# Optimization experiments

Measured on AMD Instinct MI355X. Metric: run time of the kernel, lower is better.

Reference implementation:

```python
import jax, jax.numpy as jnp
import numpy as np

B, T, C, H = 4, 1024, 1024, 16
D = C // H
EPS = 1e-5


def _ln(x, g, b):
    mu = jnp.mean(x, axis=-1, keepdims=True)
    var = jnp.mean((x - mu) ** 2, axis=-1, keepdims=True)
    return (x - mu) * jax.lax.rsqrt(var + EPS) * g + b


def _attn(xq, xkv, wq, wk, wv, wo, bo, mask):
    # wq/wk/wv/wo: [C, C] (in, out). Dropout is identity in eval mode.
    Bq, Tq, _ = xq.shape
    Tk = xkv.shape[1]
    q = (xq @ wq).reshape(Bq, Tq, H, D)
    k = (xkv @ wk).reshape(Bq, Tk, H, D)
    v = (xkv @ wv).reshape(Bq, Tk, H, D)
    scores = jnp.einsum('bqhd,bkhd->bhqk', q, k) / jnp.sqrt(jnp.float32(D))
    if mask is not None:
        scores = jnp.where(mask == 0, -jnp.inf, scores)
    p = jax.nn.softmax(scores, axis=-1)
    out = jnp.einsum('bhqk,bkhd->bqhd', p, v).reshape(Bq, Tq, C)
    return out @ wo + bo


def setup_inputs() -> dict:
    key = jax.random.key(0)
    ks = jax.random.split(key, 20)
    s = 0.02
    inp = {
        'x': jax.random.normal(ks[0], (B, T, C), jnp.float32),
        'encoder_out': jax.random.normal(ks[1], (B, T, C), jnp.float32),
        'sa_wq': jax.random.normal(ks[2], (C, C), jnp.float32) * s,
        'sa_wk': jax.random.normal(ks[3], (C, C), jnp.float32) * s,
        'sa_wv': jax.random.normal(ks[4], (C, C), jnp.float32) * s,
        'sa_wo': jax.random.normal(ks[5], (C, C), jnp.float32) * s,
        'sa_bo': jnp.zeros((C,), jnp.float32),
        'ca_wq': jax.random.normal(ks[6], (C, C), jnp.float32) * s,
        'ca_wk': jax.random.normal(ks[7], (C, C), jnp.float32) * s,
        'ca_wv': jax.random.normal(ks[8], (C, C), jnp.float32) * s,
        'ca_wo': jax.random.normal(ks[9], (C, C), jnp.float32) * s,
        'ca_bo': jnp.zeros((C,), jnp.float32),
        'ff_w1': jax.random.normal(ks[10], (C, 4 * C), jnp.float32) * s,
        'ff_b1': jnp.zeros((4 * C,), jnp.float32),
        'ff_w2': jax.random.normal(ks[11], (4 * C, C), jnp.float32) * s,
        'ff_b2': jnp.zeros((C,), jnp.float32),
        'ln1_g': jnp.ones((C,), jnp.float32), 'ln1_b': jnp.zeros((C,), jnp.float32),
        'ln2_g': jnp.ones((C,), jnp.float32), 'ln2_b': jnp.zeros((C,), jnp.float32),
        'ln3_g': jnp.ones((C,), jnp.float32), 'ln3_b': jnp.zeros((C,), jnp.float32),
        'tgt_mask': jnp.tril(jnp.ones((T, T), jnp.int32))[None, None],  # [1,1,T,T] causal
        'src_mask': jnp.ones((B, 1, 1, T), jnp.int32),
    }
    return inp


def reference(x, encoder_out, sa_wq, sa_wk, sa_wv, sa_wo, sa_bo,
              ca_wq, ca_wk, ca_wv, ca_wo, ca_bo,
              ff_w1, ff_b1, ff_w2, ff_b2,
              ln1_g, ln1_b, ln2_g, ln2_b, ln3_g, ln3_b,
              tgt_mask, src_mask):
    # self-attention (masked) + residual
    x = x + _attn(_ln(x, ln1_g, ln1_b), _ln(x, ln1_g, ln1_b),
                  sa_wq, sa_wk, sa_wv, sa_wo, sa_bo, tgt_mask)
    # cross-attention + residual (only src_mask applied to scores)
    h = _ln(x, ln2_g, ln2_b)
    x = x + _attn(h, encoder_out, ca_wq, ca_wk, ca_wv, ca_wo, ca_bo, src_mask)
    # FFN + residual
    h = _ln(x, ln3_g, ln3_b)
    x = x + (jax.nn.relu(h @ ff_w1 + ff_b1) @ ff_w2 + ff_b2)
    return x
```

## Files before the change

kernel.cpp:

```cpp
#include <hip/hip_runtime.h>

typedef __bf16 bf16_t;
typedef __bf16 bf16x4 __attribute__((ext_vector_type(4)));
typedef __bf16 bf16x8 __attribute__((ext_vector_type(8)));
typedef float  f32x4  __attribute__((ext_vector_type(4)));

#define LN_EPS 1e-5f

__device__ __forceinline__ void g2l16(const bf16_t* g, bf16_t* l) {
    __builtin_amdgcn_global_load_lds(
        (const __attribute__((address_space(1))) void*)g,
        (__attribute__((address_space(3))) void*)l, 16, 0, 0);
}

__global__ __launch_bounds__(256) void cvt_kernel(
    const float* __restrict__ x, bf16_t* __restrict__ y)
{
    int i = blockIdx.x * 256 + threadIdx.x;
    f32x4 v = ((const f32x4*)x)[i];
    bf16x4 o = { (bf16_t)v.x, (bf16_t)v.y, (bf16_t)v.z, (bf16_t)v.w };
    ((bf16x4*)y)[i] = o;
}

struct WTBatch { const float* src[8]; bf16_t* dst[8]; };

__global__ __launch_bounds__(256) void wt_batch_kernel(WTBatch p)
{
    const int K = 1024, N = 1024;
    const float* W = p.src[blockIdx.z];
    bf16_t* Wt = p.dst[blockIdx.z];
    __shared__ float ts[64][65];
    const int n0 = blockIdx.x * 64, k0 = blockIdx.y * 64;
    const int tid = threadIdx.x;
#pragma unroll
    for (int it = 0; it < 4; ++it) {
        int f = tid + it * 256;
        int row = f >> 4, c4 = (f & 15) * 4;
        f32x4 v = *(const f32x4*)(W + (size_t)(k0 + row) * N + n0 + c4);
        ts[row][c4 + 0] = v.x; ts[row][c4 + 1] = v.y;
        ts[row][c4 + 2] = v.z; ts[row][c4 + 3] = v.w;
    }
    __syncthreads();
#pragma unroll
    for (int it = 0; it < 4; ++it) {
        int f = tid + it * 256;
        int nrow = f >> 4, k4 = (f & 15) * 4;
        bf16x4 o = { (bf16_t)ts[k4 + 0][nrow], (bf16_t)ts[k4 + 1][nrow],
                     (bf16_t)ts[k4 + 2][nrow], (bf16_t)ts[k4 + 3][nrow] };
        *(bf16x4*)(Wt + (size_t)(n0 + nrow) * K + k0 + k4) = o;
    }
}

__global__ __launch_bounds__(256) void wt_kernel(
    const float* __restrict__ W, bf16_t* __restrict__ Wt, int K, int N)
{
    __shared__ float ts[64][65];
    const int n0 = blockIdx.x * 64, k0 = blockIdx.y * 64;
    const int tid = threadIdx.x;
#pragma unroll
    for (int it = 0; it < 4; ++it) {
        int f = tid + it * 256;
        int row = f >> 4, c4 = (f & 15) * 4;
        f32x4 v = *(const f32x4*)(W + (size_t)(k0 + row) * N + n0 + c4);
        ts[row][c4 + 0] = v.x; ts[row][c4 + 1] = v.y;
        ts[row][c4 + 2] = v.z; ts[row][c4 + 3] = v.w;
    }
    __syncthreads();
#pragma unroll
    for (int it = 0; it < 4; ++it) {
        int f = tid + it * 256;
        int nrow = f >> 4, k4 = (f & 15) * 4;
        bf16x4 o = { (bf16_t)ts[k4 + 0][nrow], (bf16_t)ts[k4 + 1][nrow],
                     (bf16_t)ts[k4 + 2][nrow], (bf16_t)ts[k4 + 3][nrow] };
        *(bf16x4*)(Wt + (size_t)(n0 + nrow) * K + k0 + k4) = o;
    }
}

__global__ __launch_bounds__(256) void ln_kernel(
    const float* __restrict__ x, const float* __restrict__ g,
    const float* __restrict__ b, bf16_t* __restrict__ y)
{
    const int row = blockIdx.x;
    const int tid = threadIdx.x;
    const f32x4* xr = (const f32x4*)(x + (size_t)row * 1024);
    f32x4 v = xr[tid];
    float s  = v.x + v.y + v.z + v.w;
    float s2 = v.x*v.x + v.y*v.y + v.z*v.z + v.w*v.w;
#pragma unroll
    for (int off = 1; off < 64; off <<= 1) {
        s  += __shfl_xor(s,  off, 64);
        s2 += __shfl_xor(s2, off, 64);
    }
    __shared__ float ws_[4], ws2_[4];
    const int wave = tid >> 6, lane = tid & 63;
    if (lane == 0) { ws_[wave] = s; ws2_[wave] = s2; }
    __syncthreads();
    s  = ws_[0] + ws_[1] + ws_[2] + ws_[3];
    s2 = ws2_[0] + ws2_[1] + ws2_[2] + ws2_[3];
    const float mu   = s  * (1.0f/1024.0f);
    const float var  = s2 * (1.0f/1024.0f) - mu*mu;
    const float rstd = rsqrtf(var + LN_EPS);
    f32x4 gv = ((const f32x4*)g)[tid];
    f32x4 bv = ((const f32x4*)b)[tid];
    f32x4 o  = (v - mu) * rstd * gv + bv;
    bf16x4 ob = { (bf16_t)o.x, (bf16_t)o.y, (bf16_t)o.z, (bf16_t)o.w };
    ((bf16x4*)(y + (size_t)row * 1024))[tid] = ob;
}

template<int BN, int OUT_BF16, int HAS_BIAS, int DO_RELU, int HAS_RES>
__global__ __launch_bounds__(256) void gemm_bf16(
    const bf16_t* __restrict__ A, const bf16_t* __restrict__ Bt,
    const float* __restrict__ bias, const float* __restrict__ res,
    void* __restrict__ out, int M, int N, int K)
{
    constexpr int NT = BN / 32;
    __shared__ __align__(16) bf16_t As[2][128 * 32];
    __shared__ __align__(16) bf16_t Bs[2][BN * 32];

    const int tid  = threadIdx.x;
    const int wave = tid >> 6, lane = tid & 63;
    const int q    = lane >> 4, r = lane & 15;
    const int wm   = wave >> 1, wn = wave & 1;
    const int m0   = blockIdx.y * 128, n0 = blockIdx.x * BN;

    const int srow = lane >> 2;
    const int schk = (lane & 3) * 8;

    auto stage = [&](int buf, int kk) {
#pragma unroll
        for (int t = 0; t < 2; ++t) {
            int rowA = wave * 32 + t * 16;
            g2l16(A + (size_t)(m0 + rowA + srow) * K + kk + schk, &As[buf][rowA * 32]);
        }
        if constexpr (BN == 128) {
#pragma unroll
            for (int t = 0; t < 2; ++t) {
                int rowB = wave * 32 + t * 16;
                g2l16(Bt + (size_t)(n0 + rowB + srow) * K + kk + schk, &Bs[buf][rowB * 32]);
            }
        } else {
            int rowB = wave * 16;
            g2l16(Bt + (size_t)(n0 + rowB + srow) * K + kk + schk, &Bs[buf][rowB * 32]);
        }
    };

    f32x4 acc[4][NT] = {};
    stage(0, 0);

    for (int kk = 0; kk < K; kk += 32) {
        const int cur = (kk >> 5) & 1;
        __syncthreads();
        if (kk + 32 < K) stage(cur ^ 1, kk + 32);

        bf16x8 af[4], bf[NT];
#pragma unroll
        for (int i = 0; i < 4; ++i)
            af[i] = *(const bf16x8*)&As[cur][(wm * 64 + i * 16 + r) * 32 + q * 8];
#pragma unroll
        for (int j = 0; j < NT; ++j)
            bf[j] = *(const bf16x8*)&Bs[cur][(wn * 16 * NT + j * 16 + r) * 32 + q * 8];
#pragma unroll
        for (int i = 0; i < 4; ++i)
#pragma unroll
            for (int j = 0; j < NT; ++j)
                acc[i][j] = __builtin_amdgcn_mfma_f32_16x16x32_bf16(af[i], bf[j], acc[i][j], 0, 0, 0);
    }

#pragma unroll
    for (int i = 0; i < 4; ++i)
#pragma unroll
        for (int j = 0; j < NT; ++j)
#pragma unroll
            for (int e = 0; e < 4; ++e) {
                int row = m0 + wm * 64 + i * 16 + q * 4 + e;
                int col = n0 + wn * 16 * NT + j * 16 + r;
                float v = acc[i][j][e];
                if (HAS_BIAS) v += bias[col];
                if (DO_RELU)  v = v > 0.0f ? v : 0.0f;
                if (HAS_RES)  v += res[(size_t)row * N + col];
                if (OUT_BF16) ((bf16_t*)out)[(size_t)row * N + col] = (bf16_t)v;
                else          ((float*)out)[(size_t)row * N + col] = v;
            }
}

__global__ __launch_bounds__(256) void gemm_qkv3(
    const bf16_t* __restrict__ Aq, const bf16_t* __restrict__ Akv,
    const bf16_t* __restrict__ Wt3,
    bf16_t* __restrict__ outq, bf16_t* __restrict__ outk,
    bf16_t* __restrict__ vt)
{
    const int K = 1024;
    __shared__ __align__(16) bf16_t As[2][128 * 32];
    __shared__ __align__(16) bf16_t Bs[2][128 * 32];

    const int tid  = threadIdx.x;
    const int wave = tid >> 6, lane = tid & 63;
    const int q    = lane >> 4, r = lane & 15;
    const int wm   = wave >> 1, wn = wave & 1;
    const int m0   = blockIdx.y * 128, n0 = blockIdx.x * 128;
    const int grp  = blockIdx.x >> 3;
    const bf16_t* A = (grp == 0) ? Aq : Akv;

    const int srow = lane >> 2;
    const int schk = (lane & 3) * 8;

    auto stage = [&](int buf, int kk) {
#pragma unroll
        for (int t = 0; t < 2; ++t) {
            int row = wave * 32 + t * 16;
            g2l16(A   + (size_t)(m0 + row + srow) * K + kk + schk, &As[buf][row * 32]);
            g2l16(Wt3 + (size_t)(n0 + row + srow) * K + kk + schk, &Bs[buf][row * 32]);
        }
    };

    f32x4 acc[4][4] = {};
    stage(0, 0);

    for (int kk = 0; kk < K; kk += 32) {
        const int cur = (kk >> 5) & 1;
        __syncthreads();
        if (kk + 32 < K) stage(cur ^ 1, kk + 32);

        bf16x8 af[4], bf[4];
#pragma unroll
        for (int i = 0; i < 4; ++i)
            af[i] = *(const bf16x8*)&As[cur][(wm * 64 + i * 16 + r) * 32 + q * 8];
#pragma unroll
        for (int j = 0; j < 4; ++j)
            bf[j] = *(const bf16x8*)&Bs[cur][(wn * 64 + j * 16 + r) * 32 + q * 8];
#pragma unroll
        for (int i = 0; i < 4; ++i)
#pragma unroll
            for (int j = 0; j < 4; ++j)
                acc[i][j] = __builtin_amdgcn_mfma_f32_16x16x32_bf16(af[i], bf[j], acc[i][j], 0, 0, 0);
    }

    if (grp < 2) {
        bf16_t* o = (grp == 0) ? outq : outk;
        const int c0 = n0 - grp * 1024;
#pragma unroll
        for (int i = 0; i < 4; ++i)
#pragma unroll
            for (int j = 0; j < 4; ++j)
#pragma unroll
                for (int e = 0; e < 4; ++e) {
                    int row = m0 + wm * 64 + i * 16 + q * 4 + e;
                    int col = c0 + wn * 64 + j * 16 + r;
                    o[(size_t)row * 1024 + col] = (bf16_t)acc[i][j][e];
                }
    } else {
#pragma unroll
        for (int i = 0; i < 4; ++i)
#pragma unroll
            for (int j = 0; j < 4; ++j) {
                int c = (n0 - 2048) + wn * 64 + j * 16 + r;
                int hh = c >> 6, d = c & 63;
                int row0 = m0 + wm * 64 + i * 16 + q * 4;
                int bb = row0 >> 10, t = row0 & 1023;
                bf16x4 pk = { (bf16_t)acc[i][j][0], (bf16_t)acc[i][j][1],
                              (bf16_t)acc[i][j][2], (bf16_t)acc[i][j][3] };
                *(bf16x4*)&vt[((size_t)((bb << 4) + hh) * 64 + d) * 1024 + t] = pk;
            }
    }
}

template<int CAUSAL>
__global__ __launch_bounds__(256) void attn_mfma_kernel(
    const bf16_t* __restrict__ Qp, const bf16_t* __restrict__ Kp,
    const bf16_t* __restrict__ VTp, bf16_t* __restrict__ Op)
{
    const int T = 1024;
    const int LP = 72;
    __shared__ __align__(16) bf16_t Ps[128 * LP];
    __shared__ __align__(16) bf16_t Ks[2][2][64 * 32];
    __shared__ __align__(16) bf16_t Vs[2][2][64 * 32];

    const int qt = blockIdx.x, h = blockIdx.y, b = blockIdx.z;
    const int tid  = threadIdx.x;
    const int wave = tid >> 6, lane = tid & 63;
    const int q    = lane >> 4, r = lane & 15;
    const int srow = lane >> 2, schk = (lane & 3) * 8;

    const bf16_t* Kb = Kp + (size_t)(b * T) * 1024 + h * 64;
    const bf16_t* Vb = VTp + (size_t)((b * 16 + h) * 64) * 1024;

    auto stageKV = [&](int buf, int kt) {
#pragma unroll
        for (int ks = 0; ks < 2; ++ks) {
            g2l16(Kb + (size_t)(kt * 64 + wave * 16 + srow) * 1024 + ks * 32 + schk,
                  &Ks[buf][ks][wave * 16 * 32]);
            g2l16(Vb + (size_t)(wave * 16 + srow) * 1024 + kt * 64 + ks * 32 + schk,
                  &Vs[buf][ks][wave * 16 * 32]);
        }
    };

    {
        const bf16_t* Qb = Qp + (size_t)(b * T + qt * 128) * 1024 + h * 64;
#pragma unroll
        for (int it = 0; it < 4; ++it) {
            int f = tid + it * 256;
            int row = f >> 3, c8 = (f & 7) * 8;
            *(bf16x8*)&Ps[row * LP + c8] = *(const bf16x8*)(Qb + (size_t)row * 1024 + c8);
        }
    }
    __syncthreads();
    bf16x8 qa[2][2];
#pragma unroll
    for (int mt = 0; mt < 2; ++mt)
#pragma unroll
        for (int ks = 0; ks < 2; ++ks)
            qa[mt][ks] = *(const bf16x8*)&Ps[(wave * 32 + mt * 16 + r) * LP + ks * 32 + q * 8];

    f32x4 m_prev[2], l_run[2];
    f32x4 o[2][4] = {};
#pragma unroll
    for (int mt = 0; mt < 2; ++mt)
#pragma unroll
        for (int i2 = 0; i2 < 4; ++i2) { m_prev[mt][i2] = -INFINITY; l_run[mt][i2] = 0.0f; }

    const int nk = CAUSAL ? (2 * qt + 2) : 16;
    stageKV(0, 0);

    for (int kt = 0; kt < nk; ++kt) {
        const int cur = kt & 1;
        __syncthreads();
        if (kt + 1 < nk) stageKV(cur ^ 1, kt + 1);

        f32x4 s[2][4] = {};
#pragma unroll
        for (int ks = 0; ks < 2; ++ks)
#pragma unroll
            for (int nt = 0; nt < 4; ++nt) {
                bf16x8 kb = *(const bf16x8*)&Ks[cur][ks][(nt * 16 + r) * 32 + q * 8];
#pragma unroll
                for (int mt = 0; mt < 2; ++mt)
                    s[mt][nt] = __builtin_amdgcn_mfma_f32_16x16x32_bf16(qa[mt][ks], kb, s[mt][nt], 0, 0, 0);
            }
#pragma unroll
        for (int mt = 0; mt < 2; ++mt)
#pragma unroll
            for (int nt = 0; nt < 4; ++nt) s[mt][nt] *= 0.125f;

        if (CAUSAL) {
#pragma unroll
            for (int mt = 0; mt < 2; ++mt) {
                const int r0 = qt * 128 + wave * 32 + mt * 16;
                if (kt * 64 + 63 > r0) {
#pragma unroll
                    for (int nt = 0; nt < 4; ++nt) {
                        int kg = kt * 64 + nt * 16 + r;
#pragma unroll
                        for (int i2 = 0; i2 < 4; ++i2)
                            if (kg > r0 + q * 4 + i2) s[mt][nt][i2] = -INFINITY;
                    }
                }
            }
        }

#pragma unroll
        for (int mt = 0; mt < 2; ++mt) {
            f32x4 mloc = s[mt][0];
#pragma unroll
            for (int nt = 1; nt < 4; ++nt)
#pragma unroll
                for (int i2 = 0; i2 < 4; ++i2) mloc[i2] = fmaxf(mloc[i2], s[mt][nt][i2]);
#pragma unroll
            for (int off = 1; off < 16; off <<= 1)
#pragma unroll
                for (int i2 = 0; i2 < 4; ++i2)
                    mloc[i2] = fmaxf(mloc[i2], __shfl_xor(mloc[i2], off, 64));

            f32x4 mnew, alpha, lsum;
#pragma unroll
            for (int i2 = 0; i2 < 4; ++i2) {
                mnew[i2]  = fmaxf(m_prev[mt][i2], mloc[i2]);
                alpha[i2] = __expf(m_prev[mt][i2] - mnew[i2]);
                lsum[i2]  = 0.0f;
            }
#pragma unroll
            for (int nt = 0; nt < 4; ++nt)
#pragma unroll
                for (int i2 = 0; i2 < 4; ++i2) {
                    float p = __expf(s[mt][nt][i2] - mnew[i2]);
                    s[mt][nt][i2] = p;
                    lsum[i2] += p;
                }
#pragma unroll
            for (int off = 1; off < 16; off <<= 1)
#pragma unroll
                for (int i2 = 0; i2 < 4; ++i2) lsum[i2] += __shfl_xor(lsum[i2], off, 64);
#pragma unroll
            for (int i2 = 0; i2 < 4; ++i2) {
                l_run[mt][i2]  = l_run[mt][i2] * alpha[i2] + lsum[i2];
                m_prev[mt][i2] = mnew[i2];
            }
#pragma unroll
            for (int nt = 0; nt < 4; ++nt)
#pragma unroll
                for (int i2 = 0; i2 < 4; ++i2) {
                    Ps[(wave * 32 + mt * 16 + q * 4 + i2) * LP + nt * 16 + r] = (bf16_t)s[mt][nt][i2];
                    o[mt][nt][i2] *= alpha[i2];
                }
        }

#pragma unroll
        for (int ks = 0; ks < 2; ++ks) {
            bf16x8 pa[2];
#pragma unroll
            for (int mt = 0; mt < 2; ++mt)
                pa[mt] = *(const bf16x8*)&Ps[(wave * 32 + mt * 16 + r) * LP + ks * 32 + q * 8];
#pragma unroll
            for (int dt = 0; dt < 4; ++dt) {
                bf16x8 vb = *(const bf16x8*)&Vs[cur][ks][(dt * 16 + r) * 32 + q * 8];
#pragma unroll
                for (int mt = 0; mt < 2; ++mt)
                    o[mt][dt] = __builtin_amdgcn_mfma_f32_16x16x32_bf16(pa[mt], vb, o[mt][dt], 0, 0, 0);
            }
        }
    }

    bf16_t* Ob = Op + (size_t)(b * T + qt * 128 + wave * 32) * 1024 + h * 64;
#pragma unroll
    for (int mt = 0; mt < 2; ++mt) {
        f32x4 inv;
#pragma unroll
        for (int i2 = 0; i2 < 4; ++i2) inv[i2] = 1.0f / l_run[mt][i2];
#pragma unroll
        for (int dt = 0; dt < 4; ++dt)
#pragma unroll
            for (int i2 = 0; i2 < 4; ++i2)
                Ob[(size_t)(mt * 16 + q * 4 + i2) * 1024 + dt * 16 + r] = (bf16_t)(o[mt][dt][i2] * inv[i2]);
    }
}

extern "C" void kernel_launch(void* const* d_in, const int* in_sizes, int n_in,
                              void* d_out, int out_size, void* d_ws, size_t ws_size,
                              hipStream_t stream)
{
    const float* x     = (const float*)d_in[0];
    const float* enc   = (const float*)d_in[1];
    const float* sa_wq = (const float*)d_in[2];
    const float* sa_wk = (const float*)d_in[3];
    const float* sa_wv = (const float*)d_in[4];
    const float* sa_wo = (const float*)d_in[5];
    const float* sa_bo = (const float*)d_in[6];
    const float* ca_wq = (const float*)d_in[7];
    const float* ca_wk = (const float*)d_in[8];
    const float* ca_wv = (const float*)d_in[9];
    const float* ca_wo = (const float*)d_in[10];
    const float* ca_bo = (const float*)d_in[11];
    const float* ff_w1 = (const float*)d_in[12];
    const float* ff_b1 = (const float*)d_in[13];
    const float* ff_w2 = (const float*)d_in[14];
    const float* ff_b2 = (const float*)d_in[15];
    const float* ln1_g = (const float*)d_in[16];
    const float* ln1_b = (const float*)d_in[17];
    const float* ln2_g = (const float*)d_in[18];
    const float* ln2_b = (const float*)d_in[19];
    const float* ln3_g = (const float*)d_in[20];
    const float* ln3_b = (const float*)d_in[21];

    float* out = (float*)d_out;
    char* ws = (char*)d_ws;
    const size_t MB = 1024 * 1024;
    bf16_t* w_s3  = (bf16_t*)(ws +  0 * MB);
    bf16_t* w_so  = (bf16_t*)(ws +  6 * MB);
    bf16_t* w_c3  = (bf16_t*)(ws +  8 * MB);
    bf16_t* w_co  = (bf16_t*)(ws + 14 * MB);
    bf16_t* w_f1  = (bf16_t*)(ws + 16 * MB);
    bf16_t* w_f2  = (bf16_t*)(ws + 24 * MB);
    bf16_t* b_enc = (bf16_t*)(ws + 32 * MB);
    bf16_t* b_ln  = (bf16_t*)(ws + 40 * MB);
    bf16_t* b_q   = (bf16_t*)(ws + 48 * MB);
    bf16_t* b_k   = (bf16_t*)(ws + 56 * MB);
    bf16_t* b_vt  = (bf16_t*)(ws + 64 * MB);
    bf16_t* b_at  = (bf16_t*)(ws + 72 * MB);
    float*  b_x1  = (float*) (ws + 80 * MB);
    float*  b_x2  = (float*) (ws + 48 * MB);
    bf16_t* b_h1  = (bf16_t*)(ws + 64 * MB);

    const int M = 4096;
    dim3 blk(256);

    WTBatch wb;
    wb.src[0] = sa_wq; wb.dst[0] = w_s3;
    wb.src[1] = sa_wk; wb.dst[1] = w_s3 + 1024 * 1024;
    wb.src[2] = sa_wv; wb.dst[2] = w_s3 + 2048 * 1024;
    wb.src[3] = sa_wo; wb.dst[3] = w_so;
    wb.src[4] = ca_wq; wb.dst[4] = w_c3;
    wb.src[5] = ca_wk; wb.dst[5] = w_c3 + 1024 * 1024;
    wb.src[6] = ca_wv; wb.dst[6] = w_c3 + 2048 * 1024;
    wb.src[7] = ca_wo; wb.dst[7] = w_co;
    wt_batch_kernel<<<dim3(16, 16, 8), blk, 0, stream>>>(wb);
    wt_kernel<<<dim3(64, 16), blk, 0, stream>>>(ff_w1, w_f1, 1024, 4096);
    wt_kernel<<<dim3(16, 64), blk, 0, stream>>>(ff_w2, w_f2, 4096, 1024);
    cvt_kernel<<<4096, blk, 0, stream>>>(enc, b_enc);

    ln_kernel<<<4096, blk, 0, stream>>>(x, ln1_g, ln1_b, b_ln);
    gemm_qkv3<<<dim3(24, 32), blk, 0, stream>>>(b_ln, b_ln, w_s3, b_q, b_k, b_vt);
    attn_mfma_kernel<1><<<dim3(8, 16, 4), blk, 0, stream>>>(b_q, b_k, b_vt, b_at);
    gemm_bf16<64,0,1,0,1><<<dim3(16, 32), blk, 0, stream>>>(
        b_at, w_so, sa_bo, x, b_x1, M, 1024, 1024);
    ln_kernel<<<4096, blk, 0, stream>>>(b_x1, ln2_g, ln2_b, b_ln);
    gemm_qkv3<<<dim3(24, 32), blk, 0, stream>>>(b_ln, b_enc, w_c3, b_q, b_k, b_vt);
    attn_mfma_kernel<0><<<dim3(8, 16, 4), blk, 0, stream>>>(b_q, b_k, b_vt, b_at);
    gemm_bf16<64,0,1,0,1><<<dim3(16, 32), blk, 0, stream>>>(
        b_at, w_co, ca_bo, b_x1, b_x2, M, 1024, 1024);
    ln_kernel<<<4096, blk, 0, stream>>>(b_x2, ln3_g, ln3_b, b_ln);
    gemm_bf16<128,1,1,1,0><<<dim3(32, 32), blk, 0, stream>>>(
        b_ln, w_f1, ff_b1, nullptr, b_h1, M, 4096, 1024);
    gemm_bf16<64,0,1,0,1><<<dim3(16, 32), blk, 0, stream>>>(
        b_h1, w_f2, ff_b2, b_x2, out, M, 1024, 4096);
}
```

Baseline: 567.0 us.

## Swizzle block order for XCD locality, deepen GEMM K-staging, merge weight transposes

Remaps block IDs in the GEMM, QKV and attention kernels so that consecutive blocks, which are spread round-robin over the 8 XCDs, map to contiguous tiles. Each XCD's L2 then sees better reuse of A and B tiles. The BN=64 GEMMs now stage two 32-wide K slices per barrier, halving the number of syncs at the cost of more LDS. All weight transposes are folded into a single 16-slice launch to cut launch overhead. The remapping assumes gridDim.y is divisible by 8 and a fixed attention grid shape.

```diff
diff --git a/kernel.cpp b/kernel.cpp
--- a/kernel.cpp
+++ b/kernel.cpp
@@ -22,15 +22,19 @@
     ((bf16x4*)y)[i] = o;
 }
 
-struct WTBatch { const float* src[8]; bf16_t* dst[8]; };
-
-__global__ __launch_bounds__(256) void wt_batch_kernel(WTBatch p)
-{
-    const int K = 1024, N = 1024;
-    const float* W = p.src[blockIdx.z];
-    bf16_t* Wt = p.dst[blockIdx.z];
+struct WT16 {
+    const float* src[16]; bf16_t* dst[16];
+    int srcN[16]; int dstK[16]; int k0b[16]; int n0b[16];
+};
+
+__global__ __launch_bounds__(256) void wt16_kernel(WT16 p)
+{
+    const int z = blockIdx.z;
+    const float* W = p.src[z];
+    bf16_t* Wt = p.dst[z];
+    const int N = p.srcN[z], Kd = p.dstK[z];
+    const int n0 = p.n0b[z] + blockIdx.x * 64, k0 = p.k0b[z] + blockIdx.y * 64;
     __shared__ float ts[64][65];
-    const int n0 = blockIdx.x * 64, k0 = blockIdx.y * 64;
     const int tid = threadIdx.x;
 #pragma unroll
     for (int it = 0; it < 4; ++it) {
@@ -47,32 +51,7 @@
         int nrow = f >> 4, k4 = (f & 15) * 4;
         bf16x4 o = { (bf16_t)ts[k4 + 0][nrow], (bf16_t)ts[k4 + 1][nrow],
                      (bf16_t)ts[k4 + 2][nrow], (bf16_t)ts[k4 + 3][nrow] };
-        *(bf16x4*)(Wt + (size_t)(n0 + nrow) * K + k0 + k4) = o;
-    }
-}
-
-__global__ __launch_bounds__(256) void wt_kernel(
-    const float* __restrict__ W, bf16_t* __restrict__ Wt, int K, int N)
-{
-    __shared__ float ts[64][65];
-    const int n0 = blockIdx.x * 64, k0 = blockIdx.y * 64;
-    const int tid = threadIdx.x;
-#pragma unroll
-    for (int it = 0; it < 4; ++it) {
-        int f = tid + it * 256;
-        int row = f >> 4, c4 = (f & 15) * 4;
-        f32x4 v = *(const f32x4*)(W + (size_t)(k0 + row) * N + n0 + c4);
-        ts[row][c4 + 0] = v.x; ts[row][c4 + 1] = v.y;
-        ts[row][c4 + 2] = v.z; ts[row][c4 + 3] = v.w;
-    }
-    __syncthreads();
-#pragma unroll
-    for (int it = 0; it < 4; ++it) {
-        int f = tid + it * 256;
-        int nrow = f >> 4, k4 = (f & 15) * 4;
-        bf16x4 o = { (bf16_t)ts[k4 + 0][nrow], (bf16_t)ts[k4 + 1][nrow],
-                     (bf16_t)ts[k4 + 2][nrow], (bf16_t)ts[k4 + 3][nrow] };
-        *(bf16x4*)(Wt + (size_t)(n0 + nrow) * K + k0 + k4) = o;
+        *(bf16x4*)(Wt + (size_t)(n0 + nrow) * Kd + k0 + k4) = o;
     }
 }
 
@@ -107,63 +86,73 @@
     ((bf16x4*)(y + (size_t)row * 1024))[tid] = ob;
 }
 
-template<int BN, int OUT_BF16, int HAS_BIAS, int DO_RELU, int HAS_RES>
+template<int BN, int DEPTH, int OUT_BF16, int HAS_BIAS, int DO_RELU, int HAS_RES>
 __global__ __launch_bounds__(256) void gemm_bf16(
     const bf16_t* __restrict__ A, const bf16_t* __restrict__ Bt,
     const float* __restrict__ bias, const float* __restrict__ res,
     void* __restrict__ out, int M, int N, int K)
 {
     constexpr int NT = BN / 32;
-    __shared__ __align__(16) bf16_t As[2][128 * 32];
-    __shared__ __align__(16) bf16_t Bs[2][BN * 32];
+    __shared__ __align__(16) bf16_t As[2][DEPTH][128 * 32];
+    __shared__ __align__(16) bf16_t Bs[2][DEPTH][BN * 32];
 
     const int tid  = threadIdx.x;
     const int wave = tid >> 6, lane = tid & 63;
     const int q    = lane >> 4, r = lane & 15;
     const int wm   = wave >> 1, wn = wave & 1;
-    const int m0   = blockIdx.y * 128, n0 = blockIdx.x * BN;
+
+    const int nbx  = gridDim.x;
+    const int id   = blockIdx.y * nbx + blockIdx.x;
+    const int mper = gridDim.y >> 3;
+    const int jj   = id >> 3;
+    const int bm   = (id & 7) * mper + jj / nbx;
+    const int bn   = jj % nbx;
+    const int m0   = bm * 128, n0 = bn * BN;
 
     const int srow = lane >> 2;
     const int schk = (lane & 3) * 8;
 
     auto stage = [&](int buf, int kk) {
 #pragma unroll
-        for (int t = 0; t < 2; ++t) {
-            int rowA = wave * 32 + t * 16;
-            g2l16(A + (size_t)(m0 + rowA + srow) * K + kk + schk, &As[buf][rowA * 32]);
-        }
-        if constexpr (BN == 128) {
+        for (int s = 0; s < DEPTH; ++s) {
 #pragma unroll
             for (int t = 0; t < 2; ++t) {
-                int rowB = wave * 32 + t * 16;
-                g2l16(Bt + (size_t)(n0 + rowB + srow) * K + kk + schk, &Bs[buf][rowB * 32]);
-            }
-        } else {
-            int rowB = wave * 16;
-            g2l16(Bt + (size_t)(n0 + rowB + srow) * K + kk + schk, &Bs[buf][rowB * 32]);
+                int rowA = wave * 32 + t * 16;
+                g2l16(A + (size_t)(m0 + rowA + srow) * K + kk + s * 32 + schk,
+                      &As[buf][s][rowA * 32]);
+            }
+#pragma unroll
+            for (int t = 0; t < BN / 64; ++t) {
+                int rowB = wave * (BN / 4) + t * 16;
+                g2l16(Bt + (size_t)(n0 + rowB + srow) * K + kk + s * 32 + schk,
+                      &Bs[buf][s][rowB * 32]);
+            }
         }
     };
 
     f32x4 acc[4][NT] = {};
+    constexpr int STEP = 32 * DEPTH;
     stage(0, 0);
 
-    for (int kk = 0; kk < K; kk += 32) {
-        const int cur = (kk >> 5) & 1;
+    for (int kk = 0; kk < K; kk += STEP) {
+        const int cur = (kk / STEP) & 1;
         __syncthreads();
-        if (kk + 32 < K) stage(cur ^ 1, kk + 32);
-
-        bf16x8 af[4], bf[NT];
-#pragma unroll
-        for (int i = 0; i < 4; ++i)
-            af[i] = *(const bf16x8*)&As[cur][(wm * 64 + i * 16 + r) * 32 + q * 8];
-#pragma unroll
-        for (int j = 0; j < NT; ++j)
-            bf[j] = *(const bf16x8*)&Bs[cur][(wn * 16 * NT + j * 16 + r) * 32 + q * 8];
-#pragma unroll
-        for (int i = 0; i < 4; ++i)
+        if (kk + STEP < K) stage(cur ^ 1, kk + STEP);
+#pragma unroll
+        for (int s = 0; s < DEPTH; ++s) {
+            bf16x8 af[4], bf[NT];
+#pragma unroll
+            for (int i = 0; i < 4; ++i)
+                af[i] = *(const bf16x8*)&As[cur][s][(wm * 64 + i * 16 + r) * 32 + q * 8];
 #pragma unroll
             for (int j = 0; j < NT; ++j)
-                acc[i][j] = __builtin_amdgcn_mfma_f32_16x16x32_bf16(af[i], bf[j], acc[i][j], 0, 0, 0);
+                bf[j] = *(const bf16x8*)&Bs[cur][s][(wn * 16 * NT + j * 16 + r) * 32 + q * 8];
+#pragma unroll
+            for (int i = 0; i < 4; ++i)
+#pragma unroll
+                for (int j = 0; j < NT; ++j)
+                    acc[i][j] = __builtin_amdgcn_mfma_f32_16x16x32_bf16(af[i], bf[j], acc[i][j], 0, 0, 0);
+        }
     }
 
 #pragma unroll
@@ -197,8 +186,15 @@
     const int wave = tid >> 6, lane = tid & 63;
     const int q    = lane >> 4, r = lane & 15;
     const int wm   = wave >> 1, wn = wave & 1;
-    const int m0   = blockIdx.y * 128, n0 = blockIdx.x * 128;
-    const int grp  = blockIdx.x >> 3;
+
+    const int nbx  = gridDim.x;
+    const int id   = blockIdx.y * nbx + blockIdx.x;
+    const int mper = gridDim.y >> 3;
+    const int jj   = id >> 3;
+    const int bm   = (id & 7) * mper + jj / nbx;
+    const int bn   = jj % nbx;
+    const int m0   = bm * 128, n0 = bn * 128;
+    const int grp  = bn >> 3;
     const bf16_t* A = (grp == 0) ? Aq : Akv;
 
     const int srow = lane >> 2;
@@ -275,7 +271,12 @@
     __shared__ __align__(16) bf16_t Ks[2][2][64 * 32];
     __shared__ __align__(16) bf16_t Vs[2][2][64 * 32];
 
-    const int qt = blockIdx.x, h = blockIdx.y, b = blockIdx.z;
+    const int id  = blockIdx.x + 8 * (blockIdx.y + 16 * blockIdx.z);
+    const int jj  = id >> 3;
+    const int pr  = (id & 7) * 8 + (jj >> 3);
+    const int qt  = jj & 7;
+    const int h   = pr & 15, b = pr >> 4;
+
     const int tid  = threadIdx.x;
     const int wave = tid >> 6, lane = tid & 63;
     const int q    = lane >> 4, r = lane & 15;
@@ -482,33 +483,38 @@
     const int M = 4096;
     dim3 blk(256);
 
-    WTBatch wb;
-    wb.src[0] = sa_wq; wb.dst[0] = w_s3;
-    wb.src[1] = sa_wk; wb.dst[1] = w_s3 + 1024 * 1024;
-    wb.src[2] = sa_wv; wb.dst[2] = w_s3 + 2048 * 1024;
-    wb.src[3] = sa_wo; wb.dst[3] = w_so;
-    wb.src[4] = ca_wq; wb.dst[4] = w_c3;
-    wb.src[5] = ca_wk; wb.dst[5] = w_c3 + 1024 * 1024;
-    wb.src[6] = ca_wv; wb.dst[6] = w_c3 + 2048 * 1024;
-    wb.src[7] = ca_wo; wb.dst[7] = w_co;
-    wt_batch_kernel<<<dim3(16, 16, 8), blk, 0, stream>>>(wb);
-    wt_kernel<<<dim3(64, 16), blk, 0, stream>>>(ff_w1, w_f1, 1024, 4096);
-    wt_kernel<<<dim3(16, 64), blk, 0, stream>>>(ff_w2, w_f2, 4096, 1024);
+    WT16 wp;
+    const float* srcs[8] = { sa_wq, sa_wk, sa_wv, sa_wo, ca_wq, ca_wk, ca_wv, ca_wo };
+    bf16_t* dsts[8] = { w_s3, w_s3 + 1024*1024, w_s3 + 2048*1024, w_so,
+                        w_c3, w_c3 + 1024*1024, w_c3 + 2048*1024, w_co };
+    for (int z = 0; z < 8; ++z) {
+        wp.src[z] = srcs[z]; wp.dst[z] = dsts[z];
+        wp.srcN[z] = 1024; wp.dstK[z] = 1024; wp.k0b[z] = 0; wp.n0b[z] = 0;
+    }
+    for (int z = 8; z < 12; ++z) {
+        wp.src[z] = ff_w1; wp.dst[z] = w_f1;
+        wp.srcN[z] = 4096; wp.dstK[z] = 1024; wp.k0b[z] = 0; wp.n0b[z] = (z - 8) * 1024;
+    }
+    for (int z = 12; z < 16; ++z) {
+        wp.src[z] = ff_w2; wp.dst[z] = w_f2;
+        wp.srcN[z] = 1024; wp.dstK[z] = 4096; wp.k0b[z] = (z - 12) * 1024; wp.n0b[z] = 0;
+    }
+    wt16_kernel<<<dim3(16, 16, 16), blk, 0, stream>>>(wp);
     cvt_kernel<<<4096, blk, 0, stream>>>(enc, b_enc);
 
     ln_kernel<<<4096, blk, 0, stream>>>(x, ln1_g, ln1_b, b_ln);
     gemm_qkv3<<<dim3(24, 32), blk, 0, stream>>>(b_ln, b_ln, w_s3, b_q, b_k, b_vt);
     attn_mfma_kernel<1><<<dim3(8, 16, 4), blk, 0, stream>>>(b_q, b_k, b_vt, b_at);
-    gemm_bf16<64,0,1,0,1><<<dim3(16, 32), blk, 0, stream>>>(
+    gemm_bf16<64,2,0,1,0,1><<<dim3(16, 32), blk, 0, stream>>>(
         b_at, w_so, sa_bo, x, b_x1, M, 1024, 1024);
     ln_kernel<<<4096, blk, 0, stream>>>(b_x1, ln2_g, ln2_b, b_ln);
     gemm_qkv3<<<dim3(24, 32), blk, 0, stream>>>(b_ln, b_enc, w_c3, b_q, b_k, b_vt);
     attn_mfma_kernel<0><<<dim3(8, 16, 4), blk, 0, stream>>>(b_q, b_k, b_vt, b_at);
-    gemm_bf16<64,0,1,0,1><<<dim3(16, 32), blk, 0, stream>>>(
+    gemm_bf16<64,2,0,1,0,1><<<dim3(16, 32), blk, 0, stream>>>(
         b_at, w_co, ca_bo, b_x1, b_x2, M, 1024, 1024);
     ln_kernel<<<4096, blk, 0, stream>>>(b_x2, ln3_g, ln3_b, b_ln);
-    gemm_bf16<128,1,1,1,0><<<dim3(32, 32), blk, 0, stream>>>(
+    gemm_bf16<128,1,1,1,1,0><<<dim3(32, 32), blk, 0, stream>>>(
         b_ln, w_f1, ff_b1, nullptr, b_h1, M, 4096, 1024);
-    gemm_bf16<64,0,1,0,1><<<dim3(16, 32), blk, 0, stream>>>(
+    gemm_bf16<64,2,0,1,0,1><<<dim3(16, 32), blk, 0, stream>>>(
         b_h1, w_f2, ff_b2, b_x2, out, M, 1024, 4096);
 }
```

New measurement: 531.4 us. 6.3% less time.
